# Performance work log

Hardware: AMD Instinct MI355X
Metric: run time of the kernel (lower is better)

Reference implementation:

```python
import jax, jax.numpy as jnp
import numpy as np

B, G, N, E, F, H = 16, 8, 512, 8192, 128, 128
BN_EPS = 1e-5


def setup_inputs() -> dict:
    key = jax.random.key(0)
    ks = jax.random.split(key, 6)
    feats = jax.random.normal(ks[0], (B, G, N, F), jnp.float32)
    edges = jax.random.randint(ks[1], (B, G, 2, E), 0, N, dtype=jnp.int32)
    s = lambda k, shape: jax.random.normal(k, shape, jnp.float32) * 0.05
    return {
        "feats": feats,
        "edges": edges,
        "W0": s(ks[2], (F, H)), "b0": jnp.zeros((H,), jnp.float32),
        "W1": s(ks[3], (H, H)), "b1": jnp.zeros((H,), jnp.float32),
        "Wt": s(ks[4], (H, H)), "bt": jnp.zeros((H,), jnp.float32),
        "gamma": jnp.ones((H,), jnp.float32),
        "beta": jnp.zeros((H,), jnp.float32),
        "run_mean": jnp.zeros((H,), jnp.float32),
        "run_var": jnp.ones((H,), jnp.float32),
    }


def _gconv(x, src, dst, W, b):
    # DGL GraphConv with norm='both': relu(D_in^{-1/2} A D_out^{-1/2} X W + b)
    ones = jnp.ones(src.shape, jnp.float32)
    out_deg = jnp.clip(jax.ops.segment_sum(ones, src, num_segments=N), 1.0)
    in_deg = jnp.clip(jax.ops.segment_sum(ones, dst, num_segments=N), 1.0)
    h = x * jax.lax.rsqrt(out_deg)[:, None]          # src normalization
    agg = jax.ops.segment_sum(h[src], dst, num_segments=N)  # SpMM gather+scatter
    h = agg * jax.lax.rsqrt(in_deg)[:, None]          # dst normalization
    return jax.nn.relu(h @ W + b)


def reference(feats, edges, W0, b0, W1, b1, Wt, bt, gamma, beta, run_mean, run_var):
    def per_graph(x, e):
        src, dst = e[0], e[1]
        h = _gconv(x, src, dst, W0, b0)
        h = _gconv(h, src, dst, W1, b1)
        emb = h.mean(axis=0)  # dgl.mean_nodes readout -> [H]
        z = emb @ Wt + bt
        # BatchNorm1d in eval mode (batch of 1 graph embedding)
        z = gamma * (z - run_mean) * jax.lax.rsqrt(run_var + BN_EPS) + beta
        return jax.nn.relu(z)

    xf = feats.reshape(B * G, N, F)
    ef = edges.reshape(B * G, 2, E)
    out = jax.vmap(per_graph)(xf, ef)  # [B*G, H]
    # torch.stack nesting gives (batch, n_graph, 1, H) since mean_nodes returns [1, H]
    return out.reshape(B, G, 1, H)
```

## Files before the change

### kernel.cpp

```cpp
#include <hip/hip_runtime.h>
#include <hip/hip_bf16.h>

#define NN 512
#define NE 8192
#define NG 128
#define FH 128
#define APITCH 68
#define XPITCH 136
#define BN_EPS 1e-5f

typedef __attribute__((ext_vector_type(8))) short s8v;
typedef __attribute__((ext_vector_type(4))) float f4v;
typedef __attribute__((ext_vector_type(16))) float f16v;
typedef __attribute__((ext_vector_type(4))) unsigned short us4v;
typedef __attribute__((ext_vector_type(4))) unsigned int u4v;

__device__ inline unsigned short f2bf(float x) {
    unsigned u = __float_as_uint(x);
    unsigned r = (u + 0x7fffu + ((u >> 16) & 1u)) >> 16;
    return (unsigned short)r;
}
__device__ inline float bf2f(unsigned short h) { return __uint_as_float(((unsigned)h) << 16); }

__device__ inline unsigned bfpack(int f1bits, int f0bits) {
    return __builtin_amdgcn_perm((unsigned)f1bits, (unsigned)f0bits, 0x07060302u);
}

__global__ __launch_bounds__(1024) void k_build(const int* __restrict__ edges,
                                                float* __restrict__ rs_out,
                                                float* __restrict__ rs_in,
                                                int* __restrict__ bofs,
                                                unsigned short* __restrict__ epk,
                                                const float* __restrict__ W0,
                                                const float* __restrict__ W1,
                                                unsigned short* __restrict__ WP) {
    int g = blockIdx.x;
    int tid = threadIdx.x;

    if (g >= NG) {
        int which = g - NG;
        if (which == 0) {
            for (int task = tid; task < 2048; task += 1024) {
                int t = task >> 6;
                int lane = task & 63;
                int nt = t >> 2, kk = t & 3;
                int n = nt * 16 + (lane & 15);
                int k0 = kk * 32 + (lane >> 4) * 8;
                unsigned short* dh = WP + ((size_t)t * 64 + lane) * 8;
                unsigned short* dl = WP + 16384 + ((size_t)t * 64 + lane) * 8;
#pragma unroll
                for (int j = 0; j < 8; j++) {
                    float v = W0[(size_t)(k0 + j) * FH + n];
                    unsigned short h = f2bf(v);
                    dh[j] = h;
                    dl[j] = f2bf(v - bf2f(h));
                }
            }
        } else {
            for (int task = tid; task < 2048; task += 1024) {
                int kk = task >> 8;
                int rem = task & 255;
                int lhp = rem >> 7, c = rem & 127;
                unsigned short* dh = WP + 2 * 16384 + ((size_t)((kk * 2 + lhp) * 128 + c)) * 8;
                unsigned short* dl = WP + 3 * 16384 + ((size_t)((kk * 2 + lhp) * 128 + c)) * 8;
#pragma unroll
                for (int j = 0; j < 8; j++) {
                    float v = W1[(size_t)(kk * 16 + lhp * 8 + j) * FH + c];
                    unsigned short h = f2bf(v);
                    dh[j] = h;
                    dl[j] = f2bf(v - bf2f(h));
                }
            }
        }
        return;
    }

    const int* src = edges + (size_t)g * 2 * NE;
    const int* dst = src + NE;

    __shared__ int degO[NN], degI[NN];
    __shared__ int scanA[1024], scanB[1024];
    __shared__ int fill[1024];
    __shared__ unsigned short pk[NE];

    for (int i = tid; i < NN; i += 1024) { degO[i] = 0; degI[i] = 0; }
    scanA[tid] = 0;
    __syncthreads();

    int rep = tid & 31;
    for (int u = tid; u < NE / 4; u += 1024) {
        int4 s = ((const int4*)src)[u];
        int4 d = ((const int4*)dst)[u];
        atomicAdd(&degO[s.x], 1); atomicAdd(&degO[s.y], 1);
        atomicAdd(&degO[s.z], 1); atomicAdd(&degO[s.w], 1);
        atomicAdd(&degI[d.x], 1); atomicAdd(&degI[d.y], 1);
        atomicAdd(&degI[d.z], 1); atomicAdd(&degI[d.w], 1);
        atomicAdd(&scanA[((((d.x >> 7) << 3) | (s.x >> 6)) << 5) + rep], 1);
        atomicAdd(&scanA[((((d.y >> 7) << 3) | (s.y >> 6)) << 5) + rep], 1);
        atomicAdd(&scanA[((((d.z >> 7) << 3) | (s.z >> 6)) << 5) + rep], 1);
        atomicAdd(&scanA[((((d.w >> 7) << 3) | (s.w >> 6)) << 5) + rep], 1);
    }
    __syncthreads();

    for (int i = tid; i < NN; i += 1024) {
        rs_out[g * NN + i] = rsqrtf((float)max(degO[i], 1));
        rs_in [g * NN + i] = rsqrtf((float)max(degI[i], 1));
    }

    int* sA = scanA; int* sB = scanB;
    for (int off = 1; off < 1024; off <<= 1) {
        int v = sA[tid];
        if (tid >= off) v += sA[tid - off];
        sB[tid] = v;
        __syncthreads();
        int* t = sA; sA = sB; sB = t;
    }
    int excl = tid ? sA[tid - 1] : 0;
    fill[tid] = excl;
    if ((tid & 31) == 0) bofs[g * 33 + (tid >> 5)] = excl;
    if (tid == 0) bofs[g * 33 + 32] = NE;
    __syncthreads();

    for (int u = tid; u < NE / 4; u += 1024) {
        int4 s = ((const int4*)src)[u];
        int4 d = ((const int4*)dst)[u];
        int c, p;
        c = ((((d.x >> 7) << 3) | (s.x >> 6)) << 5) + rep;
        p = atomicAdd(&fill[c], 1); pk[p] = (unsigned short)(((d.x & 127) << 6) | (s.x & 63));
        c = ((((d.y >> 7) << 3) | (s.y >> 6)) << 5) + rep;
        p = atomicAdd(&fill[c], 1); pk[p] = (unsigned short)(((d.y & 127) << 6) | (s.y & 63));
        c = ((((d.z >> 7) << 3) | (s.z >> 6)) << 5) + rep;
        p = atomicAdd(&fill[c], 1); pk[p] = (unsigned short)(((d.z & 127) << 6) | (s.z & 63));
        c = ((((d.w >> 7) << 3) | (s.w >> 6)) << 5) + rep;
        p = atomicAdd(&fill[c], 1); pk[p] = (unsigned short)(((d.w & 127) << 6) | (s.w & 63));
    }
    __syncthreads();
    ((int4*)(epk + (size_t)g * NE))[tid] = ((const int4*)pk)[tid];
}

__global__ __launch_bounds__(512) void k_packA(const int* __restrict__ bofs,
                                               const unsigned short* __restrict__ epk,
                                               unsigned short* __restrict__ AP) {
    int g = blockIdx.x, sb = blockIdx.y, tid = threadIdx.x;
    __shared__ float Af[128 * APITCH];
    __shared__ int bo_s[9];
    const unsigned short* ep = epk + (size_t)g * NE;
    unsigned short* Ag = AP + (size_t)g * 262144;

    if (tid < 9) bo_s[tid] = bofs[g * 33 + sb * 8 + tid];
    __syncthreads();
    int evNext = -1;
    { int e0 = bo_s[0] + tid; if (e0 < bo_s[1]) evNext = (int)ep[e0]; }

    for (int p = 0; p < 8; p++) {
        if (p) __syncthreads();
        float4 z4 = {0.f, 0.f, 0.f, 0.f};
        for (int i = tid; i < 128 * APITCH / 4; i += 512) ((float4*)Af)[i] = z4;
        __syncthreads();
        if (evNext >= 0) atomicAdd(&Af[(evNext >> 6) * APITCH + (evNext & 63)], 1.0f);
        for (int e = bo_s[p] + tid + 512; e < bo_s[p + 1]; e += 512) {
            int v = ep[e];
            atomicAdd(&Af[(v >> 6) * APITCH + (v & 63)], 1.0f);
        }
        __syncthreads();
        if (p < 7) { int e1 = bo_s[p + 1] + tid; evNext = (e1 < bo_s[p + 2]) ? (int)ep[e1] : -1; }
        else evNext = -1;
#pragma unroll
        for (int uu = 0; uu < 2; uu++) {
            int u = tid + uu * 512;
            int l31 = u & 31, lh = (u >> 5) & 1, Kl = (u >> 6) & 3, Rl = (u >> 8) & 3;
            const int4* ap = (const int4*)&Af[(Rl * 32 + l31) * APITCH + Kl * 16 + lh * 8];
            int4 a0 = ap[0], a1 = ap[1];
            u4v cv;
            cv.x = bfpack(a0.y, a0.x);
            cv.y = bfpack(a0.w, a0.z);
            cv.z = bfpack(a1.y, a1.x);
            cv.w = bfpack(a1.w, a1.z);
            int Rg = sb * 4 + Rl, K = p * 4 + Kl;
            *(u4v*)(Ag + (((size_t)(Rg * 32 + K) * 2 + lh) * 32 + l31) * 8) = cv;
        }
    }
}

__global__ __launch_bounds__(256) void k_gemm_f32(const float* __restrict__ X,
                                                  const unsigned short* __restrict__ WPh,
                                                  const unsigned short* __restrict__ WPl,
                                                  const float* __restrict__ rs,
                                                  unsigned short* __restrict__ Yf) {
    __shared__ unsigned short xh[64 * XPITCH];
    __shared__ unsigned short xl[64 * XPITCH];
    int tid = threadIdx.x;
    int sb = blockIdx.y;
    size_t r0 = (size_t)blockIdx.x * NN + (size_t)sb * 64;

    const float4* Xv = (const float4*)(X + r0 * FH);
#pragma unroll
    for (int i = 0; i < 8; i++) {
        int u = tid + i * 256;
        int row = u >> 5, c4 = (u & 31) * 4;
        float4 v = Xv[u];
        int off = row * XPITCH + c4;
        unsigned short h0 = f2bf(v.x), h1 = f2bf(v.y), h2 = f2bf(v.z), h3 = f2bf(v.w);
        us4v hv, lv;
        hv.x = h0; hv.y = h1; hv.z = h2; hv.w = h3;
        lv.x = f2bf(v.x - bf2f(h0));
        lv.y = f2bf(v.y - bf2f(h1));
        lv.z = f2bf(v.z - bf2f(h2));
        lv.w = f2bf(v.w - bf2f(h3));
        *(us4v*)(xh + off) = hv;
        *(us4v*)(xl + off) = lv;
    }
    __syncthreads();

    int lane = tid & 63, w = tid >> 6;
    int quad = lane >> 4, m = lane & 15;
    int arow = w * 16 + m;

    f4v acc[8];
#pragma unroll
    for (int nt = 0; nt < 8; nt++) acc[nt] = (f4v){0.f, 0.f, 0.f, 0.f};

#pragma unroll
    for (int kk = 0; kk < 4; kk++) {
        s8v ah = *(const s8v*)&xh[arow * XPITCH + kk * 32 + quad * 8];
        s8v al = *(const s8v*)&xl[arow * XPITCH + kk * 32 + quad * 8];
#pragma unroll
        for (int nt = 0; nt < 8; nt++) {
            s8v bh = *(const s8v*)(WPh + ((size_t)(nt * 4 + kk) * 64 + lane) * 8);
            s8v bl = *(const s8v*)(WPl + ((size_t)(nt * 4 + kk) * 64 + lane) * 8);
            acc[nt] = __builtin_amdgcn_mfma_f32_16x16x32_bf16(ah, bh, acc[nt], 0, 0, 0);
            acc[nt] = __builtin_amdgcn_mfma_f32_16x16x32_bf16(al, bh, acc[nt], 0, 0, 0);
            acc[nt] = __builtin_amdgcn_mfma_f32_16x16x32_bf16(ah, bl, acc[nt], 0, 0, 0);
        }
    }

    int orow = w * 16 + quad * 4;
    float4 rsv = *(const float4*)(rs + r0 + orow);
    int kb = sb * 4 + w, h2 = quad >> 1, j0 = (quad & 1) * 4;
    unsigned short* of = Yf + (size_t)blockIdx.x * (NN * FH);
#pragma unroll
    for (int nt = 0; nt < 8; nt++) {
        us4v v;
        v.x = f2bf(acc[nt][0] * rsv.x);
        v.y = f2bf(acc[nt][1] * rsv.y);
        v.z = f2bf(acc[nt][2] * rsv.z);
        v.w = f2bf(acc[nt][3] * rsv.w);
        *(us4v*)(of + ((size_t)(kb * 2 + h2) * 128 + nt * 16 + m) * 8 + j0) = v;
    }
}

__global__ __launch_bounds__(256, 2) void k_fused(const unsigned short* __restrict__ Y1f,
                                                  const unsigned short* __restrict__ AP,
                                                  const float* __restrict__ rs_in,
                                                  const float* __restrict__ rs_out,
                                                  const float* __restrict__ bias,
                                                  const unsigned short* __restrict__ W32h,
                                                  const unsigned short* __restrict__ W32l,
                                                  unsigned short* __restrict__ Y2f) {
    int g  = blockIdx.x;
    int sb = blockIdx.y;
    int tid = threadIdx.x;
    int lane = tid & 63, w4 = tid >> 6;
    int l31 = lane & 31, lh = lane >> 5;
    int nh = w4 >> 1, mq = w4 & 1;
    int base = sb * 128;

    __shared__ unsigned short hs[128 * XPITCH];
    __shared__ float rsin_s[128];

    if (tid < 128) rsin_s[tid] = rs_in[g * NN + base + tid];

    const unsigned short* Yg = Y1f + (size_t)g * (NN * FH);
    const unsigned short* Ag = AP + (size_t)g * 262144;
    int aoff = (sb * 4 + mq * 2) * 16384 + lh * 256 + l31 * 8;
    int boff = lh * 1024 + (nh * 64 + l31) * 8;

    f16v a00, a01, a10, a11;
#pragma unroll
    for (int i = 0; i < 16; i++) { a00[i] = 0.f; a01[i] = 0.f; a10[i] = 0.f; a11[i] = 0.f; }

    s8v aF[6][2], bF[6][2];
    auto LD = [&](int buf, int K) {
        aF[buf][0] = *(const s8v*)(Ag + aoff + K * 512);
        aF[buf][1] = *(const s8v*)(Ag + aoff + 16384 + K * 512);
        bF[buf][0] = *(const s8v*)(Yg + boff + K * 2048);
        bF[buf][1] = *(const s8v*)(Yg + boff + 256 + K * 2048);
    };
    LD(0, 0); LD(1, 1); LD(2, 2); LD(3, 3); LD(4, 4); LD(5, 5);
#pragma unroll
    for (int k = 0; k < 32; k++) {
        int cur = k % 6;
        a00 = __builtin_amdgcn_mfma_f32_32x32x16_bf16(aF[cur][0], bF[cur][0], a00, 0, 0, 0);
        a01 = __builtin_amdgcn_mfma_f32_32x32x16_bf16(aF[cur][0], bF[cur][1], a01, 0, 0, 0);
        a10 = __builtin_amdgcn_mfma_f32_32x32x16_bf16(aF[cur][1], bF[cur][0], a10, 0, 0, 0);
        a11 = __builtin_amdgcn_mfma_f32_32x32x16_bf16(aF[cur][1], bF[cur][1], a11, 0, 0, 0);
        if (k + 6 < 32) LD(cur, k + 6);
    }
    __syncthreads();

#define EPI1(ACC, Rl, t)                                                        \
    {                                                                           \
        int c = nh * 64 + (t) * 32 + l31;                                       \
        float bv = bias[c];                                                     \
        _Pragma("unroll")                                                       \
        for (int r = 0; r < 16; r++) {                                          \
            int row = (mq * 2 + (Rl)) * 32 + (r & 3) + 8 * (r >> 2) + 4 * lh;   \
            float hv = fmaxf(fmaf(rsin_s[row], (ACC)[r], bv), 0.f);             \
            hs[row * XPITCH + c] = f2bf(hv);                                    \
        }                                                                       \
    }
    EPI1(a00, 0, 0) EPI1(a01, 0, 1) EPI1(a10, 1, 0) EPI1(a11, 1, 1)
#undef EPI1
    __syncthreads();

    f16v acc2[2][2];
#pragma unroll
    for (int q = 0; q < 2; q++)
#pragma unroll
        for (int t = 0; t < 2; t++)
#pragma unroll
            for (int i = 0; i < 16; i++) acc2[q][t][i] = 0.f;

#pragma unroll
    for (int kk = 0; kk < 8; kk++) {
        s8v a0 = *(const s8v*)&hs[((mq * 2 + 0) * 32 + l31) * XPITCH + kk * 16 + lh * 8];
        s8v a1 = *(const s8v*)&hs[((mq * 2 + 1) * 32 + l31) * XPITCH + kk * 16 + lh * 8];
#pragma unroll
        for (int t = 0; t < 2; t++) {
            int c = nh * 64 + t * 32 + l31;
            s8v bh = *(const s8v*)(W32h + ((size_t)((kk * 2 + lh) * 128 + c)) * 8);
            s8v bl = *(const s8v*)(W32l + ((size_t)((kk * 2 + lh) * 128 + c)) * 8);
            acc2[0][t] = __builtin_amdgcn_mfma_f32_32x32x16_bf16(a0, bh, acc2[0][t], 0, 0, 0);
            acc2[0][t] = __builtin_amdgcn_mfma_f32_32x32x16_bf16(a0, bl, acc2[0][t], 0, 0, 0);
            acc2[1][t] = __builtin_amdgcn_mfma_f32_32x32x16_bf16(a1, bh, acc2[1][t], 0, 0, 0);
            acc2[1][t] = __builtin_amdgcn_mfma_f32_32x32x16_bf16(a1, bl, acc2[1][t], 0, 0, 0);
        }
    }

    unsigned short* of = Y2f + (size_t)g * (NN * FH);
#pragma unroll
    for (int q = 0; q < 2; q++) {
        int Rgl = mq * 2 + q;
#pragma unroll
        for (int t = 0; t < 2; t++) {
            int c = nh * 64 + t * 32 + l31;
#pragma unroll
            for (int rq = 0; rq < 4; rq++) {
                int n0 = base + Rgl * 32 + 8 * rq + 4 * lh;
                float4 rsv = *(const float4*)(rs_out + (size_t)g * NN + n0);
                int kb = n0 >> 4, lhb = (n0 >> 3) & 1, j0 = n0 & 7;
                us4v v;
                v.x = f2bf(acc2[q][t][rq * 4 + 0] * rsv.x);
                v.y = f2bf(acc2[q][t][rq * 4 + 1] * rsv.y);
                v.z = f2bf(acc2[q][t][rq * 4 + 2] * rsv.z);
                v.w = f2bf(acc2[q][t][rq * 4 + 3] * rsv.w);
                *(us4v*)(of + ((size_t)(kb * 2 + lhb) * 128 + c) * 8 + j0) = v;
            }
        }
    }
}

__global__ __launch_bounds__(256, 2) void k_gather_mean(const unsigned short* __restrict__ Y2f,
                                                        const unsigned short* __restrict__ AP,
                                                        const float* __restrict__ rs_in,
                                                        const float* __restrict__ bias,
                                                        float* __restrict__ partial) {
    int g  = blockIdx.x;
    int sb = blockIdx.y;
    int tid = threadIdx.x;
    int lane = tid & 63, w4 = tid >> 6;
    int l31 = lane & 31, lh = lane >> 5;
    int nh = w4 >> 1, mq = w4 & 1;
    int base = sb * 128;

    __shared__ float red[4 * 2 * 64];
    __shared__ float rsin_s[128];

    if (tid < 128) rsin_s[tid] = rs_in[g * NN + base + tid];

    const unsigned short* Yg = Y2f + (size_t)g * (NN * FH);
    const unsigned short* Ag = AP + (size_t)g * 262144;
    int aoff = (sb * 4 + mq * 2) * 16384 + lh * 256 + l31 * 8;
    int boff = lh * 1024 + (nh * 64 + l31) * 8;

    f16v a00, a01, a10, a11;
#pragma unroll
    for (int i = 0; i < 16; i++) { a00[i] = 0.f; a01[i] = 0.f; a10[i] = 0.f; a11[i] = 0.f; }

    s8v aF[6][2], bF[6][2];
    auto LD = [&](int buf, int K) {
        aF[buf][0] = *(const s8v*)(Ag + aoff + K * 512);
        aF[buf][1] = *(const s8v*)(Ag + aoff + 16384 + K * 512);
        bF[buf][0] = *(const s8v*)(Yg + boff + K * 2048);
        bF[buf][1] = *(const s8v*)(Yg + boff + 256 + K * 2048);
    };
    LD(0, 0); LD(1, 1); LD(2, 2); LD(3, 3); LD(4, 4); LD(5, 5);
#pragma unroll
    for (int k = 0; k < 32; k++) {
        int cur = k % 6;
        a00 = __builtin_amdgcn_mfma_f32_32x32x16_bf16(aF[cur][0], bF[cur][0], a00, 0, 0, 0);
        a01 = __builtin_amdgcn_mfma_f32_32x32x16_bf16(aF[cur][0], bF[cur][1], a01, 0, 0, 0);
        a10 = __builtin_amdgcn_mfma_f32_32x32x16_bf16(aF[cur][1], bF[cur][0], a10, 0, 0, 0);
        a11 = __builtin_amdgcn_mfma_f32_32x32x16_bf16(aF[cur][1], bF[cur][1], a11, 0, 0, 0);
        if (k + 6 < 32) LD(cur, k + 6);
    }
    __syncthreads();

#pragma unroll
    for (int t = 0; t < 2; t++) {
        int c = nh * 64 + t * 32 + l31;
        float bv = bias[c];
        float s = 0.f;
#pragma unroll
        for (int r = 0; r < 16; r++) {
            int row0 = (mq * 2 + 0) * 32 + (r & 3) + 8 * (r >> 2) + 4 * lh;
            int row1 = (mq * 2 + 1) * 32 + (r & 3) + 8 * (r >> 2) + 4 * lh;
            float v0 = (t == 0) ? a00[r] : a01[r];
            float v1 = (t == 0) ? a10[r] : a11[r];
            s += fmaxf(fmaf(rsin_s[row0], v0, bv), 0.f);
            s += fmaxf(fmaf(rsin_s[row1], v1, bv), 0.f);
        }
        red[(w4 * 2 + t) * 64 + lane] = s;
    }
    __syncthreads();
    if (tid < FH) {
        int f = tid;
        int nh2 = f >> 6, t2 = (f >> 5) & 1, cl = f & 31;
        float t = 0.f;
#pragma unroll
        for (int mqq = 0; mqq < 2; mqq++) {
            int w = nh2 * 2 + mqq;
            t += red[(w * 2 + t2) * 64 + cl] + red[(w * 2 + t2) * 64 + cl + 32];
        }
        partial[((size_t)g * 4 + sb) * FH + f] = t;
    }
}

__global__ __launch_bounds__(128) void k_head(const float* __restrict__ partial,
                                              const float* __restrict__ Wt,
                                              const float* __restrict__ bt,
                                              const float* __restrict__ gamma,
                                              const float* __restrict__ beta,
                                              const float* __restrict__ rmean,
                                              const float* __restrict__ rvar,
                                              float* __restrict__ out) {
    int g = blockIdx.x;
    int j = threadIdx.x;
    __shared__ float e[FH];
    float acc4 = 0.f;
#pragma unroll
    for (int q = 0; q < 4; q++) acc4 += partial[((size_t)g * 4 + q) * FH + j];
    e[j] = acc4 * (1.0f / (float)NN);
    __syncthreads();
    float acc = bt[j];
#pragma unroll 8
    for (int k = 0; k < FH; k++) acc += e[k] * Wt[(size_t)k * FH + j];
    float z = gamma[j] * (acc - rmean[j]) * rsqrtf(rvar[j] + BN_EPS) + beta[j];
    out[g * FH + j] = fmaxf(z, 0.f);
}

extern "C" void kernel_launch(void* const* d_in, const int* in_sizes, int n_in,
                              void* d_out, int out_size, void* d_ws, size_t ws_size,
                              hipStream_t stream) {
    const float* feats = (const float*)d_in[0];
    const int*   edges = (const int*)d_in[1];
    const float* W0    = (const float*)d_in[2];
    const float* b0    = (const float*)d_in[3];
    const float* W1    = (const float*)d_in[4];
    const float* b1    = (const float*)d_in[5];
    const float* Wt    = (const float*)d_in[6];
    const float* bt    = (const float*)d_in[7];
    const float* gamma = (const float*)d_in[8];
    const float* beta  = (const float*)d_in[9];
    const float* rmean = (const float*)d_in[10];
    const float* rvar  = (const float*)d_in[11];
    float* out = (float*)d_out;

    char* w = (char*)d_ws;
    float* rs_out  = (float*)w;   w += sizeof(float) * NG * NN;
    float* rs_in   = (float*)w;   w += sizeof(float) * NG * NN;
    int*   bofs    = (int*)w;     w += sizeof(int) * NG * 33;
    unsigned short* epk = (unsigned short*)w; w += sizeof(unsigned short) * (size_t)NG * NE;
    unsigned short* WP  = (unsigned short*)w; w += sizeof(unsigned short) * 4 * 16384;
    unsigned short* Y1  = (unsigned short*)w; w += sizeof(unsigned short) * (size_t)NG * NN * FH;
    unsigned short* Y2  = (unsigned short*)w; w += sizeof(unsigned short) * (size_t)NG * NN * FH;
    unsigned short* AP  = (unsigned short*)w; w += sizeof(unsigned short) * (size_t)NG * 262144;
    float* partial = (float*)w;   w += sizeof(float) * NG * 4 * FH;

    unsigned short* WPh0 = WP;
    unsigned short* WPl0 = WP + 16384;
    unsigned short* W32h = WP + 32768;
    unsigned short* W32l = WP + 49152;

    k_build<<<NG + 2, 1024, 0, stream>>>(edges, rs_out, rs_in, bofs, epk, W0, W1, WP);

    k_packA<<<dim3(NG, 4), 512, 0, stream>>>(bofs, epk, AP);

    k_gemm_f32<<<dim3(NG, 8), 256, 0, stream>>>(feats, WPh0, WPl0, rs_out, Y1);

    k_fused<<<dim3(NG, 4), 256, 0, stream>>>(Y1, AP, rs_in, rs_out, b0, W32h, W32l, Y2);

    k_gather_mean<<<dim3(NG, 4), 256, 0, stream>>>(Y2, AP, rs_in, b1, partial);

    k_head<<<NG, 128, 0, stream>>>(partial, Wt, bt, gamma, beta, rmean, rvar, out);

    (void)in_sizes; (void)n_in; (void)out_size; (void)ws_size;
}
```

Before: 180.4 us.

## Stage full per-graph Y matrix in LDS and use 512-thread blocks per half-graph

The two SpMM kernels (k_fused and k_gather_mean) now copy the whole 512x128 bf16 Y matrix for a graph into LDS up front, which is 128KB. Each block then covers 256 rows with 8 waves instead of 128 rows with 4 waves, halving the grid to NG x 2. B fragments are read from LDS rather than streamed from global memory, so the Y matrix is fetched twice per graph instead of four times. The cost is a serial global-to-LDS copy phase with no overlap and much larger LDS use per block, which likely limits residency to one block per CU. The head kernel now reduces two partial sums instead of four.

```diff
diff --git a/kernel.cpp b/kernel.cpp
--- a/kernel.cpp
+++ b/kernel.cpp
@@ -249,159 +249,165 @@
     }
 }
 
-__global__ __launch_bounds__(256, 2) void k_fused(const unsigned short* __restrict__ Y1f,
-                                                  const unsigned short* __restrict__ AP,
-                                                  const float* __restrict__ rs_in,
-                                                  const float* __restrict__ rs_out,
-                                                  const float* __restrict__ bias,
-                                                  const unsigned short* __restrict__ W32h,
-                                                  const unsigned short* __restrict__ W32l,
-                                                  unsigned short* __restrict__ Y2f) {
+__global__ __launch_bounds__(512) void k_fused(const unsigned short* __restrict__ Y1f,
+                                               const unsigned short* __restrict__ AP,
+                                               const float* __restrict__ rs_in,
+                                               const float* __restrict__ rs_out,
+                                               const float* __restrict__ bias,
+                                               const unsigned short* __restrict__ W32h,
+                                               const unsigned short* __restrict__ W32l,
+                                               unsigned short* __restrict__ Y2f) {
     int g  = blockIdx.x;
-    int sb = blockIdx.y;
+    int rh = blockIdx.y;
     int tid = threadIdx.x;
-    int lane = tid & 63, w4 = tid >> 6;
+    int lane = tid & 63, w8 = tid >> 6;
     int l31 = lane & 31, lh = lane >> 5;
-    int nh = w4 >> 1, mq = w4 & 1;
-    int base = sb * 128;
-
-    __shared__ unsigned short hs[128 * XPITCH];
-    __shared__ float rsin_s[128];
-
-    if (tid < 128) rsin_s[tid] = rs_in[g * NN + base + tid];
-
-    const unsigned short* Yg = Y1f + (size_t)g * (NN * FH);
+    int nh = w8 >> 2, mq = w8 & 3;
+    int R0 = rh * 256;
+
+    __shared__ unsigned short Bs[NN * FH];
+    unsigned short* hs = Bs;
+    __shared__ float rsin_s[256];
+
+    const int4* Yi4 = (const int4*)(Y1f + (size_t)g * (NN * FH));
+    int4* Bi4 = (int4*)Bs;
+#pragma unroll
+    for (int i = 0; i < 16; i++) Bi4[tid + i * 512] = Yi4[tid + i * 512];
+    if (tid < 256) rsin_s[tid] = rs_in[g * NN + R0 + tid];
+
     const unsigned short* Ag = AP + (size_t)g * 262144;
-    int aoff = (sb * 4 + mq * 2) * 16384 + lh * 256 + l31 * 8;
+    int Rg0 = rh * 8 + mq * 2;
+    int aoff = Rg0 * 16384 + lh * 256 + l31 * 8;
     int boff = lh * 1024 + (nh * 64 + l31) * 8;
+    __syncthreads();
 
     f16v a00, a01, a10, a11;
 #pragma unroll
     for (int i = 0; i < 16; i++) { a00[i] = 0.f; a01[i] = 0.f; a10[i] = 0.f; a11[i] = 0.f; }
 
-    s8v aF[6][2], bF[6][2];
+    s8v aF[6][2];
     auto LD = [&](int buf, int K) {
         aF[buf][0] = *(const s8v*)(Ag + aoff + K * 512);
         aF[buf][1] = *(const s8v*)(Ag + aoff + 16384 + K * 512);
-        bF[buf][0] = *(const s8v*)(Yg + boff + K * 2048);
-        bF[buf][1] = *(const s8v*)(Yg + boff + 256 + K * 2048);
     };
     LD(0, 0); LD(1, 1); LD(2, 2); LD(3, 3); LD(4, 4); LD(5, 5);
 #pragma unroll
     for (int k = 0; k < 32; k++) {
         int cur = k % 6;
-        a00 = __builtin_amdgcn_mfma_f32_32x32x16_bf16(aF[cur][0], bF[cur][0], a00, 0, 0, 0);
-        a01 = __builtin_amdgcn_mfma_f32_32x32x16_bf16(aF[cur][0], bF[cur][1], a01, 0, 0, 0);
-        a10 = __builtin_amdgcn_mfma_f32_32x32x16_bf16(aF[cur][1], bF[cur][0], a10, 0, 0, 0);
-        a11 = __builtin_amdgcn_mfma_f32_32x32x16_bf16(aF[cur][1], bF[cur][1], a11, 0, 0, 0);
+        s8v b0 = *(const s8v*)&Bs[k * 2048 + boff];
+        s8v b1 = *(const s8v*)&Bs[k * 2048 + boff + 256];
+        a00 = __builtin_amdgcn_mfma_f32_32x32x16_bf16(aF[cur][0], b0, a00, 0, 0, 0);
+        a01 = __builtin_amdgcn_mfma_f32_32x32x16_bf16(aF[cur][0], b1, a01, 0, 0, 0);
+        a10 = __builtin_amdgcn_mfma_f32_32x32x16_bf16(aF[cur][1], b0, a10, 0, 0, 0);
+        a11 = __builtin_amdgcn_mfma_f32_32x32x16_bf16(aF[cur][1], b1, a11, 0, 0, 0);
         if (k + 6 < 32) LD(cur, k + 6);
     }
     __syncthreads();
 
-#define EPI1(ACC, Rl, t)                                                        \
-    {                                                                           \
-        int c = nh * 64 + (t) * 32 + l31;                                       \
-        float bv = bias[c];                                                     \
-        _Pragma("unroll")                                                       \
-        for (int r = 0; r < 16; r++) {                                          \
-            int row = (mq * 2 + (Rl)) * 32 + (r & 3) + 8 * (r >> 2) + 4 * lh;   \
-            float hv = fmaxf(fmaf(rsin_s[row], (ACC)[r], bv), 0.f);             \
-            hs[row * XPITCH + c] = f2bf(hv);                                    \
-        }                                                                       \
-    }
-    EPI1(a00, 0, 0) EPI1(a01, 0, 1) EPI1(a10, 1, 0) EPI1(a11, 1, 1)
-#undef EPI1
-    __syncthreads();
-
-    f16v acc2[2][2];
-#pragma unroll
-    for (int q = 0; q < 2; q++)
-#pragma unroll
-        for (int t = 0; t < 2; t++)
-#pragma unroll
-            for (int i = 0; i < 16; i++) acc2[q][t][i] = 0.f;
-
-#pragma unroll
-    for (int kk = 0; kk < 8; kk++) {
-        s8v a0 = *(const s8v*)&hs[((mq * 2 + 0) * 32 + l31) * XPITCH + kk * 16 + lh * 8];
-        s8v a1 = *(const s8v*)&hs[((mq * 2 + 1) * 32 + l31) * XPITCH + kk * 16 + lh * 8];
+#pragma unroll
+    for (int q = 0; q < 2; q++) {
 #pragma unroll
         for (int t = 0; t < 2; t++) {
             int c = nh * 64 + t * 32 + l31;
+            float bv = bias[c];
+#pragma unroll
+            for (int r = 0; r < 16; r++) {
+                int lr = mq * 64 + q * 32 + (r & 3) + 8 * (r >> 2) + 4 * lh;
+                float v = (q == 0) ? ((t == 0) ? a00[r] : a01[r])
+                                   : ((t == 0) ? a10[r] : a11[r]);
+                float hv = fmaxf(fmaf(rsin_s[lr], v, bv), 0.f);
+                hs[lr * XPITCH + c] = f2bf(hv);
+            }
+        }
+    }
+    __syncthreads();
+
+    f16v acc2[4];
+#pragma unroll
+    for (int cb = 0; cb < 4; cb++)
+#pragma unroll
+        for (int i = 0; i < 16; i++) acc2[cb][i] = 0.f;
+
+#pragma unroll
+    for (int kk = 0; kk < 8; kk++) {
+        s8v a = *(const s8v*)&hs[(w8 * 32 + l31) * XPITCH + kk * 16 + lh * 8];
+#pragma unroll
+        for (int cb = 0; cb < 4; cb++) {
+            int c = cb * 32 + l31;
             s8v bh = *(const s8v*)(W32h + ((size_t)((kk * 2 + lh) * 128 + c)) * 8);
             s8v bl = *(const s8v*)(W32l + ((size_t)((kk * 2 + lh) * 128 + c)) * 8);
-            acc2[0][t] = __builtin_amdgcn_mfma_f32_32x32x16_bf16(a0, bh, acc2[0][t], 0, 0, 0);
-            acc2[0][t] = __builtin_amdgcn_mfma_f32_32x32x16_bf16(a0, bl, acc2[0][t], 0, 0, 0);
-            acc2[1][t] = __builtin_amdgcn_mfma_f32_32x32x16_bf16(a1, bh, acc2[1][t], 0, 0, 0);
-            acc2[1][t] = __builtin_amdgcn_mfma_f32_32x32x16_bf16(a1, bl, acc2[1][t], 0, 0, 0);
+            acc2[cb] = __builtin_amdgcn_mfma_f32_32x32x16_bf16(a, bh, acc2[cb], 0, 0, 0);
+            acc2[cb] = __builtin_amdgcn_mfma_f32_32x32x16_bf16(a, bl, acc2[cb], 0, 0, 0);
         }
     }
 
     unsigned short* of = Y2f + (size_t)g * (NN * FH);
 #pragma unroll
-    for (int q = 0; q < 2; q++) {
-        int Rgl = mq * 2 + q;
-#pragma unroll
-        for (int t = 0; t < 2; t++) {
-            int c = nh * 64 + t * 32 + l31;
-#pragma unroll
-            for (int rq = 0; rq < 4; rq++) {
-                int n0 = base + Rgl * 32 + 8 * rq + 4 * lh;
-                float4 rsv = *(const float4*)(rs_out + (size_t)g * NN + n0);
-                int kb = n0 >> 4, lhb = (n0 >> 3) & 1, j0 = n0 & 7;
-                us4v v;
-                v.x = f2bf(acc2[q][t][rq * 4 + 0] * rsv.x);
-                v.y = f2bf(acc2[q][t][rq * 4 + 1] * rsv.y);
-                v.z = f2bf(acc2[q][t][rq * 4 + 2] * rsv.z);
-                v.w = f2bf(acc2[q][t][rq * 4 + 3] * rsv.w);
-                *(us4v*)(of + ((size_t)(kb * 2 + lhb) * 128 + c) * 8 + j0) = v;
-            }
-        }
-    }
-}
-
-__global__ __launch_bounds__(256, 2) void k_gather_mean(const unsigned short* __restrict__ Y2f,
-                                                        const unsigned short* __restrict__ AP,
-                                                        const float* __restrict__ rs_in,
-                                                        const float* __restrict__ bias,
-                                                        float* __restrict__ partial) {
+    for (int cb = 0; cb < 4; cb++) {
+        int c = cb * 32 + l31;
+#pragma unroll
+        for (int rq = 0; rq < 4; rq++) {
+            int n0 = R0 + w8 * 32 + 8 * rq + 4 * lh;
+            float4 rsv = *(const float4*)(rs_out + (size_t)g * NN + n0);
+            int kb = n0 >> 4, lhb = (n0 >> 3) & 1, j0 = n0 & 7;
+            us4v v;
+            v.x = f2bf(acc2[cb][rq * 4 + 0] * rsv.x);
+            v.y = f2bf(acc2[cb][rq * 4 + 1] * rsv.y);
+            v.z = f2bf(acc2[cb][rq * 4 + 2] * rsv.z);
+            v.w = f2bf(acc2[cb][rq * 4 + 3] * rsv.w);
+            *(us4v*)(of + ((size_t)(kb * 2 + lhb) * 128 + c) * 8 + j0) = v;
+        }
+    }
+}
+
+__global__ __launch_bounds__(512) void k_gather_mean(const unsigned short* __restrict__ Y2f,
+                                                     const unsigned short* __restrict__ AP,
+                                                     const float* __restrict__ rs_in,
+                                                     const float* __restrict__ bias,
+                                                     float* __restrict__ partial) {
     int g  = blockIdx.x;
-    int sb = blockIdx.y;
+    int rh = blockIdx.y;
     int tid = threadIdx.x;
-    int lane = tid & 63, w4 = tid >> 6;
+    int lane = tid & 63, w8 = tid >> 6;
     int l31 = lane & 31, lh = lane >> 5;
-    int nh = w4 >> 1, mq = w4 & 1;
-    int base = sb * 128;
-
-    __shared__ float red[4 * 2 * 64];
-    __shared__ float rsin_s[128];
-
-    if (tid < 128) rsin_s[tid] = rs_in[g * NN + base + tid];
-
-    const unsigned short* Yg = Y2f + (size_t)g * (NN * FH);
+    int nh = w8 >> 2, mq = w8 & 3;
+    int R0 = rh * 256;
+
+    __shared__ unsigned short Bs[NN * FH];
+    float* red = (float*)Bs;
+    __shared__ float rsin_s[256];
+
+    const int4* Yi4 = (const int4*)(Y2f + (size_t)g * (NN * FH));
+    int4* Bi4 = (int4*)Bs;
+#pragma unroll
+    for (int i = 0; i < 16; i++) Bi4[tid + i * 512] = Yi4[tid + i * 512];
+    if (tid < 256) rsin_s[tid] = rs_in[g * NN + R0 + tid];
+
     const unsigned short* Ag = AP + (size_t)g * 262144;
-    int aoff = (sb * 4 + mq * 2) * 16384 + lh * 256 + l31 * 8;
+    int Rg0 = rh * 8 + mq * 2;
+    int aoff = Rg0 * 16384 + lh * 256 + l31 * 8;
     int boff = lh * 1024 + (nh * 64 + l31) * 8;
+    __syncthreads();
 
     f16v a00, a01, a10, a11;
 #pragma unroll
     for (int i = 0; i < 16; i++) { a00[i] = 0.f; a01[i] = 0.f; a10[i] = 0.f; a11[i] = 0.f; }
 
-    s8v aF[6][2], bF[6][2];
+    s8v aF[6][2];
     auto LD = [&](int buf, int K) {
         aF[buf][0] = *(const s8v*)(Ag + aoff + K * 512);
         aF[buf][1] = *(const s8v*)(Ag + aoff + 16384 + K * 512);
-        bF[buf][0] = *(const s8v*)(Yg + boff + K * 2048);
-        bF[buf][1] = *(const s8v*)(Yg + boff + 256 + K * 2048);
     };
     LD(0, 0); LD(1, 1); LD(2, 2); LD(3, 3); LD(4, 4); LD(5, 5);
 #pragma unroll
     for (int k = 0; k < 32; k++) {
         int cur = k % 6;
-        a00 = __builtin_amdgcn_mfma_f32_32x32x16_bf16(aF[cur][0], bF[cur][0], a00, 0, 0, 0);
-        a01 = __builtin_amdgcn_mfma_f32_32x32x16_bf16(aF[cur][0], bF[cur][1], a01, 0, 0, 0);
-        a10 = __builtin_amdgcn_mfma_f32_32x32x16_bf16(aF[cur][1], bF[cur][0], a10, 0, 0, 0);
-        a11 = __builtin_amdgcn_mfma_f32_32x32x16_bf16(aF[cur][1], bF[cur][1], a11, 0, 0, 0);
+        s8v b0 = *(const s8v*)&Bs[k * 2048 + boff];
+        s8v b1 = *(const s8v*)&Bs[k * 2048 + boff + 256];
+        a00 = __builtin_amdgcn_mfma_f32_32x32x16_bf16(aF[cur][0], b0, a00, 0, 0, 0);
+        a01 = __builtin_amdgcn_mfma_f32_32x32x16_bf16(aF[cur][0], b1, a01, 0, 0, 0);
+        a10 = __builtin_amdgcn_mfma_f32_32x32x16_bf16(aF[cur][1], b0, a10, 0, 0, 0);
+        a11 = __builtin_amdgcn_mfma_f32_32x32x16_bf16(aF[cur][1], b1, a11, 0, 0, 0);
         if (k + 6 < 32) LD(cur, k + 6);
     }
     __syncthreads();
@@ -413,14 +419,14 @@
         float s = 0.f;
 #pragma unroll
         for (int r = 0; r < 16; r++) {
-            int row0 = (mq * 2 + 0) * 32 + (r & 3) + 8 * (r >> 2) + 4 * lh;
-            int row1 = (mq * 2 + 1) * 32 + (r & 3) + 8 * (r >> 2) + 4 * lh;
+            int lr0 = mq * 64 + 0  + (r & 3) + 8 * (r >> 2) + 4 * lh;
+            int lr1 = mq * 64 + 32 + (r & 3) + 8 * (r >> 2) + 4 * lh;
             float v0 = (t == 0) ? a00[r] : a01[r];
             float v1 = (t == 0) ? a10[r] : a11[r];
-            s += fmaxf(fmaf(rsin_s[row0], v0, bv), 0.f);
-            s += fmaxf(fmaf(rsin_s[row1], v1, bv), 0.f);
-        }
-        red[(w4 * 2 + t) * 64 + lane] = s;
+            s += fmaxf(fmaf(rsin_s[lr0], v0, bv), 0.f);
+            s += fmaxf(fmaf(rsin_s[lr1], v1, bv), 0.f);
+        }
+        red[(w8 * 2 + t) * 64 + lane] = s;
     }
     __syncthreads();
     if (tid < FH) {
@@ -428,11 +434,11 @@
         int nh2 = f >> 6, t2 = (f >> 5) & 1, cl = f & 31;
         float t = 0.f;
 #pragma unroll
-        for (int mqq = 0; mqq < 2; mqq++) {
-            int w = nh2 * 2 + mqq;
+        for (int mqq = 0; mqq < 4; mqq++) {
+            int w = nh2 * 4 + mqq;
             t += red[(w * 2 + t2) * 64 + cl] + red[(w * 2 + t2) * 64 + cl + 32];
         }
-        partial[((size_t)g * 4 + sb) * FH + f] = t;
+        partial[((size_t)g * 2 + rh) * FH + f] = t;
     }
 }
 
@@ -447,10 +453,8 @@
     int g = blockIdx.x;
     int j = threadIdx.x;
     __shared__ float e[FH];
-    float acc4 = 0.f;
-#pragma unroll
-    for (int q = 0; q < 4; q++) acc4 += partial[((size_t)g * 4 + q) * FH + j];
-    e[j] = acc4 * (1.0f / (float)NN);
+    float acc2 = partial[((size_t)g * 2 + 0) * FH + j] + partial[((size_t)g * 2 + 1) * FH + j];
+    e[j] = acc2 * (1.0f / (float)NN);
     __syncthreads();
     float acc = bt[j];
 #pragma unroll 8
@@ -485,7 +489,7 @@
     unsigned short* Y1  = (unsigned short*)w; w += sizeof(unsigned short) * (size_t)NG * NN * FH;
     unsigned short* Y2  = (unsigned short*)w; w += sizeof(unsigned short) * (size_t)NG * NN * FH;
     unsigned short* AP  = (unsigned short*)w; w += sizeof(unsigned short) * (size_t)NG * 262144;
-    float* partial = (float*)w;   w += sizeof(float) * NG * 4 * FH;
+    float* partial = (float*)w;   w += sizeof(float) * NG * 2 * FH;
 
     unsigned short* WPh0 = WP;
     unsigned short* WPl0 = WP + 16384;
@@ -498,9 +502,9 @@
 
     k_gemm_f32<<<dim3(NG, 8), 256, 0, stream>>>(feats, WPh0, WPl0, rs_out, Y1);
 
-    k_fused<<<dim3(NG, 4), 256, 0, stream>>>(Y1, AP, rs_in, rs_out, b0, W32h, W32l, Y2);
-
-    k_gather_mean<<<dim3(NG, 4), 256, 0, stream>>>(Y2, AP, rs_in, b1, partial);
+    k_fused<<<dim3(NG, 2), 512, 0, stream>>>(Y1, AP, rs_in, rs_out, b0, W32h, W32l, Y2);
+
+    k_gather_mean<<<dim3(NG, 2), 512, 0, stream>>>(Y2, AP, rs_in, b1, partial);
 
     k_head<<<NG, 128, 0, stream>>>(partial, Wt, bt, gamma, beta, rmean, rvar, out);
 
```

New measurement: 176.7 us. -2.1%, faster.
